# Kernel optimization log

Measured on AMD Instinct MI355X. Metric: run time of the kernel, lower is better.

Reference implementation:

```python
import jax, jax.numpy as jnp
import numpy as np

S, B, I, H = 2048, 128, 128, 128


def setup_inputs() -> dict:
    key = jax.random.key(0)
    k1, k2, k3, k4, k5 = jax.random.split(key, 5)
    x = jax.random.normal(k1, (S, B, I), dtype=jnp.float32)
    V = jax.random.normal(k2, (4 * H, I), dtype=jnp.float32) * 0.05
    W = jax.random.normal(k3, (4 * H, H), dtype=jnp.float32) * 0.05
    b = jax.random.normal(k4, (4 * H,), dtype=jnp.float32) * 0.05
    b2 = jax.random.normal(k5, (4 * H,), dtype=jnp.float32) * 0.05
    return {"x": x, "V": V, "W": W, "b": b, "b2": b2}


def reference(x, V, W, b, b2):
    seq_len, batch, _ = x.shape
    hid = W.shape[1]
    # Precompute input contribution for all timesteps (same math, batched matmul)
    xg = jnp.einsum('sbi,gi->sbg', x, V) + b + b2  # (S, B, 4H)

    def step(carry, xg_t):
        h, c = carry
        gates = xg_t + h @ W.T  # (B, 4H)
        i, f, g, o = jnp.split(gates, 4, axis=1)
        i = jax.nn.sigmoid(i)
        f = jax.nn.sigmoid(f)
        g = jnp.tanh(g)
        o = jax.nn.sigmoid(o)
        c = f * c + i * g
        h = o * jnp.tanh(c)
        return (h, c), h

    h0 = jnp.zeros((batch, hid), dtype=x.dtype)
    c0 = jnp.zeros((batch, hid), dtype=x.dtype)
    (h_T, c_T), hs = jax.lax.scan(step, (h0, c0), xg)  # hs: (S, B, H)
    # Original torch.cat of h_t.unsqueeze(1) along dim 0 -> (S*B, 1, H)
    h_seq = hs.reshape(seq_len * batch, 1, hid)
    return h_seq, h_T[:, None, :], c_T[:, None, :]
```

## Files before the change

### kernel.cpp

```cpp
#include <hip/hip_runtime.h>
#include <hip/hip_bf16.h>
#include <hip/hip_fp16.h>


#define S_LEN 2048
#define BATCH 128
#define HID   128
#define G4    512

typedef _Float16 h2_t __attribute__((ext_vector_type(2)));
typedef _Float16 h8_t __attribute__((ext_vector_type(8)));
typedef float    f4_t __attribute__((ext_vector_type(4)));

__global__ __launch_bounds__(256, 2)
void xg_gemm(const float* __restrict__ x, const float* __restrict__ V,
             const float* __restrict__ b, const float* __restrict__ b2,
             __half* __restrict__ xg)
{
    __shared__ h8_t As[128 * 16];
    __shared__ h8_t Bs[128 * 16];

    const int t  = threadIdx.x;
    const int m0 = blockIdx.y * 128;
    const int n0 = blockIdx.x * 128;

#pragma unroll
    for (int r = 0; r < 8; ++r) {
        int id  = t + 256 * r;
        int row = id >> 4;
        int j   = id & 15;
        const float4* gx = (const float4*)(x + (long)(m0 + row) * 128 + j * 8);
        float4 a0 = gx[0], a1 = gx[1];
        h8_t ha = { (_Float16)a0.x, (_Float16)a0.y, (_Float16)a0.z, (_Float16)a0.w,
                    (_Float16)a1.x, (_Float16)a1.y, (_Float16)a1.z, (_Float16)a1.w };
        As[row * 16 + (j ^ (row & 15))] = ha;
        const float4* gv = (const float4*)(V + (long)(n0 + row) * 128 + j * 8);
        float4 b0 = gv[0], b1 = gv[1];
        h8_t hb = { (_Float16)b0.x, (_Float16)b0.y, (_Float16)b0.z, (_Float16)b0.w,
                    (_Float16)b1.x, (_Float16)b1.y, (_Float16)b1.z, (_Float16)b1.w };
        Bs[row * 16 + (j ^ (row & 15))] = hb;
    }
    __syncthreads();

    const int w    = t >> 6;
    const int lane = t & 63;
    const int m    = lane & 15;
    const int quad = lane >> 4;

    f4_t acc[2][8];
#pragma unroll
    for (int i = 0; i < 2; ++i)
#pragma unroll
        for (int j = 0; j < 8; ++j) acc[i][j] = (f4_t)0.f;

#pragma unroll
    for (int ks = 0; ks < 4; ++ks) {
        int ch = ks * 4 + quad;
        h8_t a0 = As[(w * 32      + m) * 16 + (ch ^ m)];
        h8_t a1 = As[(w * 32 + 16 + m) * 16 + (ch ^ m)];
#pragma unroll
        for (int nt = 0; nt < 8; ++nt) {
            h8_t bf = Bs[(nt * 16 + m) * 16 + (ch ^ m)];
            acc[0][nt] = __builtin_amdgcn_mfma_f32_16x16x32_f16(a0, bf, acc[0][nt], 0, 0, 0);
            acc[1][nt] = __builtin_amdgcn_mfma_f32_16x16x32_f16(a1, bf, acc[1][nt], 0, 0, 0);
        }
    }

#pragma unroll
    for (int nt = 0; nt < 8; ++nt) {
        int col = n0 + nt * 16 + m;
        float bias = b[col] + b2[col];
#pragma unroll
        for (int mi = 0; mi < 2; ++mi) {
#pragma unroll
            for (int rg = 0; rg < 4; ++rg) {
                long mrow = (long)(m0 + w * 32 + mi * 16 + quad * 4 + rg);
                xg[mrow * G4 + col] = __float2half(acc[mi][nt][rg] + bias);
            }
        }
    }
}

__device__ __forceinline__ float fsig(float x) {
    return __builtin_amdgcn_rcpf(1.f + __expf(-x));
}
__device__ __forceinline__ float ftanh(float x) {
    return 1.f - 2.f * __builtin_amdgcn_rcpf(1.f + __expf(2.f * x));
}
__device__ __forceinline__ void bar() {
    asm volatile("s_waitcnt lgkmcnt(0)" ::: "memory");
    __builtin_amdgcn_s_barrier();
    asm volatile("" ::: "memory");
}
__device__ __forceinline__ h2_t f2h2(float f) {
    union { float f; h2_t h; } u; u.f = f; return u.h;
}

#if __has_builtin(__builtin_amdgcn_fdot2)
#define FDOT2(a, b, c) __builtin_amdgcn_fdot2((a), (b), (c), false)
#else
__device__ __forceinline__ float FDOT2(h2_t a, h2_t b, float c) {
    return c + (float)a[0] * (float)b[0] + (float)a[1] * (float)b[1];
}
#endif

__global__ __launch_bounds__(512, 2)
void lstm_scan(const __half* __restrict__ xg, const float* __restrict__ W,
               float* __restrict__ out)
{
    const int bidx = blockIdx.x;
    const int t    = threadIdx.x;
    const int kh   = t & 1;
    const int rb   = t >> 1;
    const int n0   = rb;
    const int n1   = rb + 256;

    __shared__ __align__(16) __half h_lds[HID];
    __shared__ float gates[G4];

    h2_t w0[32], w1[32];
    {
        const float4* W0 = (const float4*)(W + n0 * 128 + kh * 64);
        const float4* W1 = (const float4*)(W + n1 * 128 + kh * 64);
#pragma unroll
        for (int q = 0; q < 16; ++q) {
            float4 v = W0[q];
            w0[2 * q]     = h2_t{ (_Float16)v.x, (_Float16)v.y };
            w0[2 * q + 1] = h2_t{ (_Float16)v.z, (_Float16)v.w };
        }
#pragma unroll
        for (int q = 0; q < 16; ++q) {
            float4 v = W1[q];
            w1[2 * q]     = h2_t{ (_Float16)v.x, (_Float16)v.y };
            w1[2 * q + 1] = h2_t{ (_Float16)v.z, (_Float16)v.w };
        }
    }

    if (t < HID) h_lds[t] = __float2half(0.f);
    float c = 0.f, hlast = 0.f;
    __syncthreads();

    const int myrow = kh ? n1 : n0;
    const __half* xgp = xg + (long)bidx * G4 + myrow;
    const long step_stride = (long)BATCH * G4;

    float p0 = __half2float(xgp[0]);
    float p1 = __half2float(xgp[step_stride]);

    const bool use_tanh = (kh == 1) && (rb < 128);
    float* out_h = out + (long)bidx * HID;
    const long SBH = (long)S_LEN * BATCH * HID;

    for (int s = 0; s < S_LEN; ++s) {
        long soff = (long)((s + 2 < S_LEN) ? s + 2 : S_LEN - 1) * step_stride;
        float nx = __half2float(xgp[soff]);
        float xv = p0;

        const float4* hp = (const float4*)h_lds + kh * 8;
        float acc0 = 0.f, acc1 = 0.f;
#pragma unroll
        for (int q = 0; q < 8; ++q) {
            float4 hv = hp[q];
            h2_t ha = f2h2(hv.x), hb = f2h2(hv.y), hc = f2h2(hv.z), hd = f2h2(hv.w);
            acc0 = FDOT2(w0[4 * q],     ha, acc0);
            acc0 = FDOT2(w0[4 * q + 1], hb, acc0);
            acc0 = FDOT2(w0[4 * q + 2], hc, acc0);
            acc0 = FDOT2(w0[4 * q + 3], hd, acc0);
            acc1 = FDOT2(w1[4 * q],     ha, acc1);
            acc1 = FDOT2(w1[4 * q + 1], hb, acc1);
            acc1 = FDOT2(w1[4 * q + 2], hc, acc1);
            acc1 = FDOT2(w1[4 * q + 3], hd, acc1);
        }
        float full0 = acc0 + __shfl_xor(acc0, 1);
        float full1 = acc1 + __shfl_xor(acc1, 1);
        float full  = (kh ? full1 : full0) + xv;

        float xx  = use_tanh ? 2.f * full : full;
        float sg  = fsig(xx);
        float act = use_tanh ? 2.f * sg - 1.f : sg;
        gates[myrow] = act;
        bar();

        if (t < HID) {
            float gi = gates[t];
            float gf = gates[t + 128];
            float gg = gates[t + 256];
            float go = gates[t + 384];
            c = gf * c + gi * gg;
            float h = go * ftanh(c);
            hlast = h;
            h_lds[t] = __float2half(h);
            out_h[(long)s * (BATCH * HID) + t] = h;
        }
        bar();

        p0 = p1; p1 = nx;
    }

    if (t < HID) {
        out[SBH + (long)bidx * HID + t]                     = hlast;
        out[SBH + (long)BATCH * HID + (long)bidx * HID + t] = c;
    }
}

extern "C" void kernel_launch(void* const* d_in, const int* in_sizes, int n_in,
                              void* d_out, int out_size, void* d_ws, size_t ws_size,
                              hipStream_t stream) {
    const float* x  = (const float*)d_in[0];
    const float* V  = (const float*)d_in[1];
    const float* W  = (const float*)d_in[2];
    const float* b  = (const float*)d_in[3];
    const float* b2 = (const float*)d_in[4];
    float* out = (float*)d_out;
    __half* xg = (__half*)d_ws;

    dim3 g1(G4 / 128, (S_LEN * BATCH) / 128);
    xg_gemm<<<g1, dim3(256), 0, stream>>>(x, V, b, b2, xg);
    lstm_scan<<<dim3(BATCH), dim3(512), 0, stream>>>(xg, W, out);
}
```

Before: 1.531 ms.

## Remap LSTM scan so a quad owns one hidden unit, reduce via DPP

Each group of four lanes now owns one hidden index and computes all four gate rows over a quarter of the K dimension. The partial sums are reduced and the gates broadcast with DPP quad permutes, so the gates LDS array and one of the two barriers per timestep go away. The h buffer is double-buffered in LDS so a single barrier is enough per step. Each thread now keeps 64 packed weight registers and does 64 fdot2 per step. Per-step latency should drop, at the cost of redundant cell-state math in all four lanes of each quad.

```diff
diff --git a/kernel.cpp b/kernel.cpp
--- a/kernel.cpp
+++ b/kernel.cpp
@@ -92,9 +92,6 @@
     __builtin_amdgcn_s_barrier();
     asm volatile("" ::: "memory");
 }
-__device__ __forceinline__ h2_t f2h2(float f) {
-    union { float f; h2_t h; } u; u.f = f; return u.h;
-}
 
 #if __has_builtin(__builtin_amdgcn_fdot2)
 #define FDOT2(a, b, c) __builtin_amdgcn_fdot2((a), (b), (c), false)
@@ -103,6 +100,23 @@
     return c + (float)a[0] * (float)b[0] + (float)a[1] * (float)b[1];
 }
 #endif
+
+template <int CTRL>
+__device__ __forceinline__ float dpp_mov_f(float x) {
+#if __has_builtin(__builtin_amdgcn_mov_dpp)
+    int xi = __builtin_bit_cast(int, x);
+    int yi = __builtin_amdgcn_mov_dpp(xi, CTRL, 0xf, 0xf, true);
+    return __builtin_bit_cast(float, yi);
+#else
+    return x;
+#endif
+}
+#define QP_XOR1  0xB1
+#define QP_XOR2  0x4E
+#define QP_BC0   0x00
+#define QP_BC1   0x55
+#define QP_BC2   0xAA
+#define QP_BC3   0xFF
 
 __global__ __launch_bounds__(512, 2)
 void lstm_scan(const __half* __restrict__ xg, const float* __restrict__ W,
@@ -110,44 +124,34 @@
 {
     const int bidx = blockIdx.x;
     const int t    = threadIdx.x;
-    const int kh   = t & 1;
-    const int rb   = t >> 1;
-    const int n0   = rb;
-    const int n1   = rb + 256;
-
-    __shared__ __align__(16) __half h_lds[HID];
-    __shared__ float gates[G4];
-
-    h2_t w0[32], w1[32];
-    {
-        const float4* W0 = (const float4*)(W + n0 * 128 + kh * 64);
-        const float4* W1 = (const float4*)(W + n1 * 128 + kh * 64);
-#pragma unroll
-        for (int q = 0; q < 16; ++q) {
-            float4 v = W0[q];
-            w0[2 * q]     = h2_t{ (_Float16)v.x, (_Float16)v.y };
-            w0[2 * q + 1] = h2_t{ (_Float16)v.z, (_Float16)v.w };
-        }
-#pragma unroll
-        for (int q = 0; q < 16; ++q) {
-            float4 v = W1[q];
-            w1[2 * q]     = h2_t{ (_Float16)v.x, (_Float16)v.y };
-            w1[2 * q + 1] = h2_t{ (_Float16)v.z, (_Float16)v.w };
-        }
-    }
-
-    if (t < HID) h_lds[t] = __float2half(0.f);
-    float c = 0.f, hlast = 0.f;
+    const int hid  = t >> 2;
+    const int kq   = t & 3;
+
+    __shared__ __align__(16) __half h_buf[2][HID];
+
+    h2_t wr[4][16];
+#pragma unroll
+    for (int r = 0; r < 4; ++r) {
+        const float4* Wp = (const float4*)(W + (long)(hid + 128 * r) * 128 + kq * 32);
+#pragma unroll
+        for (int q = 0; q < 8; ++q) {
+            float4 v = Wp[q];
+            wr[r][2 * q]     = h2_t{ (_Float16)v.x, (_Float16)v.y };
+            wr[r][2 * q + 1] = h2_t{ (_Float16)v.z, (_Float16)v.w };
+        }
+    }
+
+    if (t < HID) h_buf[0][t] = __float2half(0.f);
     __syncthreads();
 
-    const int myrow = kh ? n1 : n0;
-    const __half* xgp = xg + (long)bidx * G4 + myrow;
+    const __half* xgp = xg + (long)bidx * G4 + hid + kq * 128;
     const long step_stride = (long)BATCH * G4;
 
     float p0 = __half2float(xgp[0]);
     float p1 = __half2float(xgp[step_stride]);
 
-    const bool use_tanh = (kh == 1) && (rb < 128);
+    float c = 0.f, hlast = 0.f;
+    const float ascale = (kq == 2) ? 2.f : 1.f;
     float* out_h = out + (long)bidx * HID;
     const long SBH = (long)S_LEN * BATCH * HID;
 
@@ -156,50 +160,55 @@
         float nx = __half2float(xgp[soff]);
         float xv = p0;
 
-        const float4* hp = (const float4*)h_lds + kh * 8;
-        float acc0 = 0.f, acc1 = 0.f;
-#pragma unroll
-        for (int q = 0; q < 8; ++q) {
-            float4 hv = hp[q];
-            h2_t ha = f2h2(hv.x), hb = f2h2(hv.y), hc = f2h2(hv.z), hd = f2h2(hv.w);
-            acc0 = FDOT2(w0[4 * q],     ha, acc0);
-            acc0 = FDOT2(w0[4 * q + 1], hb, acc0);
-            acc0 = FDOT2(w0[4 * q + 2], hc, acc0);
-            acc0 = FDOT2(w0[4 * q + 3], hd, acc0);
-            acc1 = FDOT2(w1[4 * q],     ha, acc1);
-            acc1 = FDOT2(w1[4 * q + 1], hb, acc1);
-            acc1 = FDOT2(w1[4 * q + 2], hc, acc1);
-            acc1 = FDOT2(w1[4 * q + 3], hd, acc1);
-        }
-        float full0 = acc0 + __shfl_xor(acc0, 1);
-        float full1 = acc1 + __shfl_xor(acc1, 1);
-        float full  = (kh ? full1 : full0) + xv;
-
-        float xx  = use_tanh ? 2.f * full : full;
-        float sg  = fsig(xx);
-        float act = use_tanh ? 2.f * sg - 1.f : sg;
-        gates[myrow] = act;
+        const float4* hp = (const float4*)(&h_buf[s & 1][0]);
+        float acc0 = 0.f, acc1 = 0.f, acc2 = 0.f, acc3 = 0.f;
+#pragma unroll
+        for (int q = 0; q < 4; ++q) {
+            union { float4 f; h2_t h[4]; } u;
+            u.f = hp[kq * 4 + q];
+#pragma unroll
+            for (int j = 0; j < 4; ++j) {
+                h2_t hh = u.h[j];
+                int cidx = q * 4 + j;
+                acc0 = FDOT2(wr[0][cidx], hh, acc0);
+                acc1 = FDOT2(wr[1][cidx], hh, acc1);
+                acc2 = FDOT2(wr[2][cidx], hh, acc2);
+                acc3 = FDOT2(wr[3][cidx], hh, acc3);
+            }
+        }
+        acc0 += dpp_mov_f<QP_XOR1>(acc0);  acc0 += dpp_mov_f<QP_XOR2>(acc0);
+        acc1 += dpp_mov_f<QP_XOR1>(acc1);  acc1 += dpp_mov_f<QP_XOR2>(acc1);
+        acc2 += dpp_mov_f<QP_XOR1>(acc2);  acc2 += dpp_mov_f<QP_XOR2>(acc2);
+        acc3 += dpp_mov_f<QP_XOR1>(acc3);  acc3 += dpp_mov_f<QP_XOR2>(acc3);
+
+        float mydot = acc0;
+        mydot = (kq == 1) ? acc1 : mydot;
+        mydot = (kq == 2) ? acc2 : mydot;
+        mydot = (kq == 3) ? acc3 : mydot;
+        float pre = mydot + xv;
+        float act = ascale * fsig(ascale * pre) - (ascale - 1.f);
+
+        float gi = dpp_mov_f<QP_BC0>(act);
+        float gf = dpp_mov_f<QP_BC1>(act);
+        float gg = dpp_mov_f<QP_BC2>(act);
+        float go = dpp_mov_f<QP_BC3>(act);
+
+        c = gf * c + gi * gg;
+        float h = go * ftanh(c);
+        hlast = h;
+
+        if (kq == 0) {
+            h_buf[(s + 1) & 1][hid] = __float2half(h);
+            out_h[(long)s * (BATCH * HID) + hid] = h;
+        }
         bar();
 
-        if (t < HID) {
-            float gi = gates[t];
-            float gf = gates[t + 128];
-            float gg = gates[t + 256];
-            float go = gates[t + 384];
-            c = gf * c + gi * gg;
-            float h = go * ftanh(c);
-            hlast = h;
-            h_lds[t] = __float2half(h);
-            out_h[(long)s * (BATCH * HID) + t] = h;
-        }
-        bar();
-
         p0 = p1; p1 = nx;
     }
 
-    if (t < HID) {
-        out[SBH + (long)bidx * HID + t]                     = hlast;
-        out[SBH + (long)BATCH * HID + (long)bidx * HID + t] = c;
+    if (kq == 0) {
+        out[SBH + (long)bidx * HID + hid]                     = hlast;
+        out[SBH + (long)BATCH * HID + (long)bidx * HID + hid] = c;
     }
 }
 
```

After: 1.434 ms. 6.3% less time.
